# Kernel optimization log

Hardware: AMD Instinct MI355X
Metric: run time of the kernel (lower is better)

The kernel has to match this reference:

```python
import jax, jax.numpy as jnp
import numpy as np

D_MODEL = 1024
NUM_HEADS = 16
HEAD_DIM = D_MODEL // NUM_HEADS


def setup_inputs() -> dict:
    key = jax.random.key(0)
    ks = jax.random.split(key, 10)
    B, SQ, SKV = 4, 2048, 2048
    s = 1.0 / np.sqrt(D_MODEL)
    return {
        "query": jax.random.normal(ks[0], (B, SQ, D_MODEL), jnp.float32),
        "key_value": jax.random.normal(ks[1], (B, SKV, D_MODEL), jnp.float32),
        "Wq": jax.random.normal(ks[2], (D_MODEL, D_MODEL), jnp.float32) * s,
        "bq": jnp.zeros((D_MODEL,), jnp.float32),
        "Wk": jax.random.normal(ks[3], (D_MODEL, D_MODEL), jnp.float32) * s,
        "bk": jnp.zeros((D_MODEL,), jnp.float32),
        "Wv": jax.random.normal(ks[4], (D_MODEL, D_MODEL), jnp.float32) * s,
        "bv": jnp.zeros((D_MODEL,), jnp.float32),
        "Wo": jax.random.normal(ks[5], (D_MODEL, D_MODEL), jnp.float32) * s,
        "bo": jnp.zeros((D_MODEL,), jnp.float32),
    }


def reference(query, key_value, Wq, bq, Wk, bk, Wv, bv, Wo, bo):
    B, SQ, _ = query.shape
    SKV = key_value.shape[1]
    H, Dh = NUM_HEADS, HEAD_DIM
    # projections (torch Linear: x @ W.T + b); split heads -> (B, H, S, Dh)
    Q = (query @ Wq.T + bq).reshape(B, SQ, H, Dh).transpose(0, 2, 1, 3)
    K = (key_value @ Wk.T + bk).reshape(B, SKV, H, Dh).transpose(0, 2, 1, 3)
    V = (key_value @ Wv.T + bv).reshape(B, SKV, H, Dh).transpose(0, 2, 1, 3)
    scale = jnp.asarray(np.sqrt(Dh), query.dtype)
    scores = jnp.einsum("bhqd,bhkd->bhqk", Q, K) / scale
    weights = jax.nn.softmax(scores, axis=-1)  # dropout is identity in eval
    attn = jnp.einsum("bhqk,bhkd->bhqd", weights, V)
    attn = attn.transpose(0, 2, 1, 3).reshape(B, SQ, H * Dh)
    return attn @ Wo.T + bo
```

## Files before the change

### kernel.cpp

```cpp
#include <hip/hip_runtime.h>

#define NH 16
#define DH 64
#define DM 1024
#define SEQ 2048
#define BATCH 4

typedef short s16x8 __attribute__((ext_vector_type(8)));
typedef float f32x4 __attribute__((ext_vector_type(4)));

__device__ __forceinline__ unsigned short f2bf(float f) {
  union { float f; unsigned int u; } v; v.f = f;
  unsigned int u = v.u;
  unsigned int r = (u + 0x7fffu + ((u >> 16) & 1u)) >> 16;
  return (unsigned short)r;
}

__device__ __forceinline__ unsigned int pkbf(float a, float b) {
#if __has_builtin(__builtin_amdgcn_cvt_pk_bf16_f32)
  typedef short v2s __attribute__((ext_vector_type(2)));
  v2s r = __builtin_amdgcn_cvt_pk_bf16_f32(a, b);
  union { v2s v; unsigned int u; } cv; cv.v = r;
  return cv.u;
#else
  return (unsigned int)f2bf(a) | ((unsigned int)f2bf(b) << 16);
#endif
}

__device__ __forceinline__ float fexp2(float x) {
#if __has_builtin(__builtin_amdgcn_exp2f)
  return __builtin_amdgcn_exp2f(x);
#else
  return exp2f(x);
#endif
}

__device__ __forceinline__ void gload_lds16(const void* g, void* l) {
  __builtin_amdgcn_global_load_lds(
      (const __attribute__((address_space(1))) unsigned int*)g,
      (__attribute__((address_space(3))) unsigned int*)l, 16, 0, 0);
}

__global__ void convert_all(const float* __restrict__ q, const float* __restrict__ kv,
                            const float* __restrict__ w0, const float* __restrict__ w1,
                            const float* __restrict__ w2, const float* __restrict__ w3,
                            unsigned short* __restrict__ oq, unsigned short* __restrict__ okv,
                            unsigned short* __restrict__ ow0, unsigned short* __restrict__ ow1,
                            unsigned short* __restrict__ ow2, unsigned short* __restrict__ ow3) {
  const int NQ4 = (BATCH * SEQ * DM) / 4;
  const int NW4 = (DM * DM) / 4;
  const int total = NQ4 * 2 + NW4 * 4;
  for (int i = blockIdx.x * blockDim.x + threadIdx.x; i < total;
       i += gridDim.x * blockDim.x) {
    const float* s; unsigned short* d; int off;
    if (i < NQ4)            { s = q;  d = oq;  off = i; }
    else if (i < 2 * NQ4)   { s = kv; d = okv; off = i - NQ4; }
    else {
      int j = i - 2 * NQ4; int wsel = j / NW4; off = j - wsel * NW4;
      s = (wsel == 0) ? w0 : (wsel == 1) ? w1 : (wsel == 2) ? w2 : w3;
      d = (wsel == 0) ? ow0 : (wsel == 1) ? ow1 : (wsel == 2) ? ow2 : ow3;
    }
    float4 v = *(const float4*)(s + (size_t)off * 4);
    ushort4 o;
    o.x = f2bf(v.x); o.y = f2bf(v.y); o.z = f2bf(v.z); o.w = f2bf(v.w);
    *(ushort4*)(d + (size_t)off * 4) = o;
  }
}

__device__ __forceinline__ void gemm_tile(const unsigned short* __restrict__ X,
                                          const unsigned short* __restrict__ Wt,
                                          unsigned short* As, unsigned short* Bs,
                                          int m0, int n0, f32x4 (*acc)[4]) {
  const int tid = threadIdx.x;
  const int wv_ = tid >> 6, lane = tid & 63;
  const int quad = lane >> 4, c = lane & 15;
  const int wm = (wv_ >> 1) * 64, wn = (wv_ & 1) * 64;
  const int srow = lane >> 3;
  const int scol = ((lane & 7) ^ srow) * 8;

  for (int kt = 0; kt < DM; kt += 64) {
#pragma unroll
    for (int i = 0; i < 4; ++i) {
      int reg = wv_ * 4 + i;
      gload_lds16(X + (size_t)(m0 + reg * 8 + srow) * DM + kt + scol,
                  (void*)(As + reg * 512));
      gload_lds16(Wt + (size_t)(n0 + reg * 8 + srow) * DM + kt + scol,
                  (void*)(Bs + reg * 512));
    }
    __syncthreads();
#pragma unroll
    for (int k2 = 0; k2 < 2; ++k2) {
      s16x8 a[4], b[4];
      int g = k2 * 4 + quad;
#pragma unroll
      for (int t = 0; t < 4; ++t)
        a[t] = *(const s16x8*)(As + (wm + t * 16 + c) * 64 + ((g ^ (c & 7)) * 8));
#pragma unroll
      for (int t = 0; t < 4; ++t)
        b[t] = *(const s16x8*)(Bs + (wn + t * 16 + c) * 64 + ((g ^ (c & 7)) * 8));
#pragma unroll
      for (int tm = 0; tm < 4; ++tm)
#pragma unroll
        for (int tn = 0; tn < 4; ++tn)
          acc[tm][tn] = __builtin_amdgcn_mfma_f32_16x16x32_bf16(
              a[tm], b[tn], acc[tm][tn], 0, 0, 0);
    }
    __syncthreads();
  }
}

__global__ __launch_bounds__(256)
void gemm_qkv(const unsigned short* __restrict__ Xq,
              const unsigned short* __restrict__ Xkv,
              const unsigned short* __restrict__ W0,
              const unsigned short* __restrict__ W1,
              const unsigned short* __restrict__ W2,
              const float* __restrict__ b0, const float* __restrict__ b1,
              const float* __restrict__ b2,
              unsigned short* __restrict__ OQ, unsigned short* __restrict__ OK_,
              unsigned short* __restrict__ OV) {
  __shared__ alignas(16) unsigned short As[128 * 64];
  __shared__ alignas(16) unsigned short Bs[128 * 64];
  const int m0 = blockIdx.x * 128;
  const int ysel = blockIdx.y >> 3;
  const int n0 = (blockIdx.y & 7) * 128;
  const unsigned short* X = (ysel == 0) ? Xq : Xkv;
  const unsigned short* Wt = (ysel == 0) ? W0 : (ysel == 1) ? W1 : W2;
  const float* bias = (ysel == 0) ? b0 : (ysel == 1) ? b1 : b2;
  unsigned short* Out = (ysel == 0) ? OQ : (ysel == 1) ? OK_ : OV;
  const float scale = (ysel == 0) ? 0.1803368801f : 1.0f;

  f32x4 acc[4][4] = {};
  gemm_tile(X, Wt, As, Bs, m0, n0, acc);

  const int tid = threadIdx.x;
  const int wv_ = tid >> 6, lane = tid & 63;
  const int quad = lane >> 4, c = lane & 15;
  const int wm = (wv_ >> 1) * 64, wn = (wv_ & 1) * 64;
#pragma unroll
  for (int tm = 0; tm < 4; ++tm) {
#pragma unroll
    for (int tn = 0; tn < 4; ++tn) {
      int n = n0 + wn + tn * 16 + c;
      float bv = bias[n];
      int m_base = m0 + wm + tm * 16 + quad * 4;
      if (ysel == 2) {
        int b_ = m_base >> 11, s_ = m_base & 2047, h_ = n >> 6, dh = n & 63;
        size_t idx = (((size_t)(b_ * NH + h_)) * DH + dh) * SEQ + s_;
        ushort4 o4;
        o4.x = f2bf(acc[tm][tn][0] + bv);
        o4.y = f2bf(acc[tm][tn][1] + bv);
        o4.z = f2bf(acc[tm][tn][2] + bv);
        o4.w = f2bf(acc[tm][tn][3] + bv);
        *(ushort4*)(&Out[idx]) = o4;
      } else {
#pragma unroll
        for (int p = 0; p < 4; ++p) {
          int m = m_base + p;
          float val = (acc[tm][tn][p] + bv) * scale;
          int b_ = m >> 11, s_ = m & 2047, h_ = n >> 6, dh = n & 63;
          size_t idx = (((size_t)(b_ * NH + h_)) * SEQ + s_) * DH + dh;
          Out[idx] = f2bf(val);
        }
      }
    }
  }
}

__global__ __launch_bounds__(256)
void gemm_o(const unsigned short* __restrict__ X,
            const unsigned short* __restrict__ Wt,
            const float* __restrict__ bias, float* __restrict__ Out) {
  __shared__ alignas(16) unsigned short As[128 * 64];
  __shared__ alignas(16) unsigned short Bs[128 * 64];
  const int m0 = blockIdx.x * 128;
  const int n0 = blockIdx.y * 128;
  f32x4 acc[4][4] = {};
  gemm_tile(X, Wt, As, Bs, m0, n0, acc);

  const int tid = threadIdx.x;
  const int wv_ = tid >> 6, lane = tid & 63;
  const int quad = lane >> 4, c = lane & 15;
  const int wm = (wv_ >> 1) * 64, wn = (wv_ & 1) * 64;
#pragma unroll
  for (int tm = 0; tm < 4; ++tm) {
#pragma unroll
    for (int tn = 0; tn < 4; ++tn) {
      int n = n0 + wn + tn * 16 + c;
      float bv = bias[n];
#pragma unroll
      for (int p = 0; p < 4; ++p) {
        int m = m0 + wm + tm * 16 + quad * 4 + p;
        Out[(size_t)m * DM + n] = acc[tm][tn][p] + bv;
      }
    }
  }
}

__global__ __launch_bounds__(256, 2)
void attn_kernel(const unsigned short* __restrict__ Qb,
                 const unsigned short* __restrict__ Kb,
                 const unsigned short* __restrict__ VTb,
                 unsigned short* __restrict__ Ob) {
  __shared__ alignas(16) unsigned short SM[16384];

  const int tid = threadIdx.x, wv_ = tid >> 6, lane = tid & 63;
  const int quad = lane >> 4, c = lane & 15;
  const int bh = blockIdx.x, qb = blockIdx.y;
  const unsigned short* Qp = Qb + (size_t)bh * SEQ * DH;
  const unsigned short* Kp = Kb + (size_t)bh * SEQ * DH;
  const unsigned short* Vp = VTb + (size_t)bh * DH * SEQ;
  const int wq0 = qb * 256 + wv_ * 64;

  s16x8 aq[4][2];
#pragma unroll
  for (int t = 0; t < 4; ++t)
#pragma unroll
    for (int k2 = 0; k2 < 2; ++k2)
      aq[t][k2] = *(const s16x8*)(Qp + (size_t)(wq0 + t * 16 + c) * DH +
                                  k2 * 32 + quad * 8);

  f32x4 ot[4][4] = {};
  float lsum[4] = {};

  const int srow = lane >> 3;
  const int schunk = (lane & 7) ^ srow;

#pragma unroll
  for (int i = 0; i < 2; ++i) {
    int reg = wv_ * 2 + i;
    gload_lds16(Kp + (size_t)(reg * 8 + srow) * DH + schunk * 8,
                (void*)(SM + reg * 512));
    gload_lds16(Vp + (size_t)(reg * 8 + srow) * SEQ + schunk * 8,
                (void*)(SM + 8192 + reg * 512));
  }

  for (int kt = 0; kt < SEQ; kt += 64) {
    const int cur = (kt >> 6) & 1;
    __syncthreads();
    if (kt + 64 < SEQ) {
      const int nxt = cur ^ 1;
#pragma unroll
      for (int i = 0; i < 2; ++i) {
        int reg = wv_ * 2 + i;
        gload_lds16(Kp + (size_t)(kt + 64 + reg * 8 + srow) * DH + schunk * 8,
                    (void*)(SM + nxt * 4096 + reg * 512));
        gload_lds16(Vp + (size_t)(reg * 8 + srow) * SEQ + kt + 64 + schunk * 8,
                    (void*)(SM + 8192 + nxt * 4096 + reg * 512));
      }
    }
    const unsigned short* K_ = SM + cur * 4096;
    const unsigned short* V_ = SM + 8192 + cur * 4096;

    f32x4 s[4][2][2] = {};
#pragma unroll
    for (int k2 = 0; k2 < 2; ++k2) {
      s16x8 ak[2][2];
#pragma unroll
      for (int jp = 0; jp < 2; ++jp)
#pragma unroll
        for (int h = 0; h < 2; ++h) {
          int r = jp * 32 + ((c >> 2) << 3) + h * 4 + (c & 3);
          int g = k2 * 4 + quad;
          ak[jp][h] = *(const s16x8*)(K_ + r * 64 + ((g ^ (r & 7)) * 8));
        }
#pragma unroll
      for (int t = 0; t < 4; ++t)
#pragma unroll
        for (int jp = 0; jp < 2; ++jp)
#pragma unroll
          for (int h = 0; h < 2; ++h)
            s[t][jp][h] = __builtin_amdgcn_mfma_f32_16x16x32_bf16(
                ak[jp][h], aq[t][k2], s[t][jp][h], 0, 0, 0);
    }

    s16x8 bp[4][2];
#pragma unroll
    for (int t = 0; t < 4; ++t)
#pragma unroll
      for (int jp = 0; jp < 2; ++jp) {
        float e00 = fexp2(s[t][jp][0][0]);
        float e01 = fexp2(s[t][jp][0][1]);
        float e02 = fexp2(s[t][jp][0][2]);
        float e03 = fexp2(s[t][jp][0][3]);
        float e10 = fexp2(s[t][jp][1][0]);
        float e11 = fexp2(s[t][jp][1][1]);
        float e12 = fexp2(s[t][jp][1][2]);
        float e13 = fexp2(s[t][jp][1][3]);
        lsum[t] += ((e00 + e01) + (e02 + e03)) + ((e10 + e11) + (e12 + e13));
        union { s16x8 v; unsigned int u[4]; } pk;
        pk.u[0] = pkbf(e00, e01);
        pk.u[1] = pkbf(e02, e03);
        pk.u[2] = pkbf(e10, e11);
        pk.u[3] = pkbf(e12, e13);
        bp[t][jp] = pk.v;
      }

#pragma unroll
    for (int jp = 0; jp < 2; ++jp)
#pragma unroll
      for (int dt = 0; dt < 4; ++dt) {
        int g = jp * 4 + quad;
        int r = dt * 16 + c;
        s16x8 av = *(const s16x8*)(V_ + r * 64 + ((g ^ (r & 7)) * 8));
#pragma unroll
        for (int t = 0; t < 4; ++t)
          ot[dt][t] = __builtin_amdgcn_mfma_f32_16x16x32_bf16(
              av, bp[t][jp], ot[dt][t], 0, 0, 0);
      }
  }

#pragma unroll
  for (int t = 0; t < 4; ++t) {
    lsum[t] += __shfl_xor(lsum[t], 16);
    lsum[t] += __shfl_xor(lsum[t], 32);
  }

  __syncthreads();

  const int b_ = bh >> 4, h_ = bh & 15;
  const int ql = lane >> 1, hf = lane & 1;
  unsigned short* Lq = SM + wv_ * (32 * 72);
#pragma unroll
  for (int half = 0; half < 2; ++half) {
    if (half) asm volatile("s_waitcnt lgkmcnt(0)" ::: "memory");
#pragma unroll
    for (int t2 = 0; t2 < 2; ++t2) {
      int t = half * 2 + t2;
      float inv = 1.0f / lsum[t];
#pragma unroll
      for (int dt = 0; dt < 4; ++dt) {
        unsigned int w01 = pkbf(ot[dt][t][0] * inv, ot[dt][t][1] * inv);
        unsigned int w23 = pkbf(ot[dt][t][2] * inv, ot[dt][t][3] * inv);
        unsigned short* p = Lq + (t2 * 16 + c) * 72 + dt * 16 + quad * 4;
        *(unsigned int*)(p) = w01;
        *(unsigned int*)(p + 2) = w23;
      }
    }
    const unsigned short* Lr = Lq + ql * 72 + hf * 32;
    unsigned short* Og = Ob + ((size_t)(b_ * SEQ + wq0 + half * 32 + ql)) * DM +
                         h_ * 64 + hf * 32;
#pragma unroll
    for (int j = 0; j < 4; ++j) {
      s16x8 v = *(const s16x8*)(Lr + j * 8);
      *(s16x8*)(Og + j * 8) = v;
    }
  }
}

extern "C" void kernel_launch(void* const* d_in, const int* in_sizes, int n_in,
                              void* d_out, int out_size, void* d_ws, size_t ws_size,
                              hipStream_t stream) {
  const float* q  = (const float*)d_in[0];
  const float* kv = (const float*)d_in[1];
  const float* Wq = (const float*)d_in[2];
  const float* bq = (const float*)d_in[3];
  const float* Wk = (const float*)d_in[4];
  const float* bk = (const float*)d_in[5];
  const float* Wv = (const float*)d_in[6];
  const float* bv = (const float*)d_in[7];
  const float* Wo = (const float*)d_in[8];
  const float* bo = (const float*)d_in[9];

  char* ws = (char*)d_ws;
  const size_t MB = 1024 * 1024;
  unsigned short* q_bf  = (unsigned short*)(ws);
  unsigned short* kv_bf = (unsigned short*)(ws + 16 * MB);
  unsigned short* wq_bf = (unsigned short*)(ws + 32 * MB);
  unsigned short* wk_bf = (unsigned short*)(ws + 34 * MB);
  unsigned short* wv_bf = (unsigned short*)(ws + 36 * MB);
  unsigned short* wo_bf = (unsigned short*)(ws + 38 * MB);
  unsigned short* Qb    = (unsigned short*)(ws + 40 * MB);
  unsigned short* Kb    = (unsigned short*)(ws + 56 * MB);
  unsigned short* VTb   = (unsigned short*)(ws + 72 * MB);
  unsigned short* attn  = (unsigned short*)(ws + 88 * MB);

  convert_all<<<2048, 256, 0, stream>>>(q, kv, Wq, Wk, Wv, Wo,
                                        q_bf, kv_bf, wq_bf, wk_bf, wv_bf, wo_bf);
  gemm_qkv<<<dim3(64, 24), 256, 0, stream>>>(q_bf, kv_bf, wq_bf, wk_bf, wv_bf,
                                             bq, bk, bv, Qb, Kb, VTb);
  attn_kernel<<<dim3(64, 8), 256, 0, stream>>>(Qb, Kb, VTb, attn);
  gemm_o<<<dim3(64, 8), 256, 0, stream>>>(attn, wo_bf, bo, (float*)d_out);
}
```

Before: 308.4 us.

## Remap workgroups per XCD, use 512-thread attention blocks, MFMA row sums

Launches the GEMM and attention kernels on 1-D grids and remaps workgroup IDs so that consecutive tiles sharing the same inputs land on the same XCD, aiming for better L2 reuse. The attention kernel now uses 512-thread blocks, each handling 512 queries, so every K/V tile loaded into shared memory serves twice as many query rows. Within a block, waves split the K and V loads by slab. The softmax row sum is now computed with an extra MFMA against a ones vector instead of scalar adds and cross-lane shuffles, which sums the bf16-rounded probabilities. The costs are higher register pressure under the new 512-thread launch bounds and a larger shared-memory array.

```diff
diff --git a/kernel.cpp b/kernel.cpp
--- a/kernel.cpp
+++ b/kernel.cpp
@@ -121,9 +121,12 @@
               unsigned short* __restrict__ OV) {
   __shared__ alignas(16) unsigned short As[128 * 64];
   __shared__ alignas(16) unsigned short Bs[128 * 64];
-  const int m0 = blockIdx.x * 128;
-  const int ysel = blockIdx.y >> 3;
-  const int n0 = (blockIdx.y & 7) * 128;
+  const int wg = blockIdx.x;
+  const int L = (wg & 7) * 192 + (wg >> 3);
+  const int m0 = (L & 63) * 128;
+  const int yy = L >> 6;
+  const int ysel = yy >> 3;
+  const int n0 = (yy & 7) * 128;
   const unsigned short* X = (ysel == 0) ? Xq : Xkv;
   const unsigned short* Wt = (ysel == 0) ? W0 : (ysel == 1) ? W1 : W2;
   const float* bias = (ysel == 0) ? b0 : (ysel == 1) ? b1 : b2;
@@ -173,8 +176,10 @@
             const float* __restrict__ bias, float* __restrict__ Out) {
   __shared__ alignas(16) unsigned short As[128 * 64];
   __shared__ alignas(16) unsigned short Bs[128 * 64];
-  const int m0 = blockIdx.x * 128;
-  const int n0 = blockIdx.y * 128;
+  const int wg = blockIdx.x;
+  const int L = (wg & 7) * 64 + (wg >> 3);
+  const int m0 = (L & 63) * 128;
+  const int n0 = (L >> 6) * 128;
   f32x4 acc[4][4] = {};
   gemm_tile(X, Wt, As, Bs, m0, n0, acc);
 
@@ -197,20 +202,22 @@
   }
 }
 
-__global__ __launch_bounds__(256, 2)
+__global__ __launch_bounds__(512, 2)
 void attn_kernel(const unsigned short* __restrict__ Qb,
                  const unsigned short* __restrict__ Kb,
                  const unsigned short* __restrict__ VTb,
                  unsigned short* __restrict__ Ob) {
-  __shared__ alignas(16) unsigned short SM[16384];
+  __shared__ alignas(16) unsigned short SM[18432];
 
   const int tid = threadIdx.x, wv_ = tid >> 6, lane = tid & 63;
   const int quad = lane >> 4, c = lane & 15;
-  const int bh = blockIdx.x, qb = blockIdx.y;
+  const int wg = blockIdx.x;
+  const int bh = (wg & 7) + 8 * ((wg >> 3) >> 2);
+  const int qb = (wg >> 3) & 3;
   const unsigned short* Qp = Qb + (size_t)bh * SEQ * DH;
   const unsigned short* Kp = Kb + (size_t)bh * SEQ * DH;
   const unsigned short* Vp = VTb + (size_t)bh * DH * SEQ;
-  const int wq0 = qb * 256 + wv_ * 64;
+  const int wq0 = qb * 512 + wv_ * 64;
 
   s16x8 aq[4][2];
 #pragma unroll
@@ -221,18 +228,29 @@
                                   k2 * 32 + quad * 8);
 
   f32x4 ot[4][4] = {};
-  float lsum[4] = {};
+  f32x4 lacc[4] = {};
+  s16x8 ones;
+  {
+    union { s16x8 v; unsigned short u[8]; } o_;
+#pragma unroll
+    for (int j = 0; j < 8; ++j) o_.u[j] = 0x3F80;
+    ones = o_.v;
+  }
 
   const int srow = lane >> 3;
   const int schunk = (lane & 7) ^ srow;
 
 #pragma unroll
   for (int i = 0; i < 2; ++i) {
-    int reg = wv_ * 2 + i;
-    gload_lds16(Kp + (size_t)(reg * 8 + srow) * DH + schunk * 8,
-                (void*)(SM + reg * 512));
-    gload_lds16(Vp + (size_t)(reg * 8 + srow) * SEQ + schunk * 8,
-                (void*)(SM + 8192 + reg * 512));
+    int slab = wv_ * 2 + i;
+    if (slab < 8) {
+      gload_lds16(Kp + (size_t)(slab * 8 + srow) * DH + schunk * 8,
+                  (void*)(SM + slab * 512));
+    } else {
+      int s2 = slab - 8;
+      gload_lds16(Vp + (size_t)(s2 * 8 + srow) * SEQ + schunk * 8,
+                  (void*)(SM + 8192 + s2 * 512));
+    }
   }
 
   for (int kt = 0; kt < SEQ; kt += 64) {
@@ -242,11 +260,15 @@
       const int nxt = cur ^ 1;
 #pragma unroll
       for (int i = 0; i < 2; ++i) {
-        int reg = wv_ * 2 + i;
-        gload_lds16(Kp + (size_t)(kt + 64 + reg * 8 + srow) * DH + schunk * 8,
-                    (void*)(SM + nxt * 4096 + reg * 512));
-        gload_lds16(Vp + (size_t)(reg * 8 + srow) * SEQ + kt + 64 + schunk * 8,
-                    (void*)(SM + 8192 + nxt * 4096 + reg * 512));
+        int slab = wv_ * 2 + i;
+        if (slab < 8) {
+          gload_lds16(Kp + (size_t)(kt + 64 + slab * 8 + srow) * DH + schunk * 8,
+                      (void*)(SM + nxt * 4096 + slab * 512));
+        } else {
+          int s2 = slab - 8;
+          gload_lds16(Vp + (size_t)(s2 * 8 + srow) * SEQ + kt + 64 + schunk * 8,
+                      (void*)(SM + 8192 + nxt * 4096 + s2 * 512));
+        }
       }
     }
     const unsigned short* K_ = SM + cur * 4096;
@@ -287,13 +309,14 @@
         float e11 = fexp2(s[t][jp][1][1]);
         float e12 = fexp2(s[t][jp][1][2]);
         float e13 = fexp2(s[t][jp][1][3]);
-        lsum[t] += ((e00 + e01) + (e02 + e03)) + ((e10 + e11) + (e12 + e13));
         union { s16x8 v; unsigned int u[4]; } pk;
         pk.u[0] = pkbf(e00, e01);
         pk.u[1] = pkbf(e02, e03);
         pk.u[2] = pkbf(e10, e11);
         pk.u[3] = pkbf(e12, e13);
         bp[t][jp] = pk.v;
+        lacc[t] = __builtin_amdgcn_mfma_f32_16x16x32_bf16(
+            ones, bp[t][jp], lacc[t], 0, 0, 0);
       }
 
 #pragma unroll
@@ -310,12 +333,6 @@
       }
   }
 
-#pragma unroll
-  for (int t = 0; t < 4; ++t) {
-    lsum[t] += __shfl_xor(lsum[t], 16);
-    lsum[t] += __shfl_xor(lsum[t], 32);
-  }
-
   __syncthreads();
 
   const int b_ = bh >> 4, h_ = bh & 15;
@@ -327,7 +344,7 @@
 #pragma unroll
     for (int t2 = 0; t2 < 2; ++t2) {
       int t = half * 2 + t2;
-      float inv = 1.0f / lsum[t];
+      float inv = 1.0f / lacc[t][0];
 #pragma unroll
       for (int dt = 0; dt < 4; ++dt) {
         unsigned int w01 = pkbf(ot[dt][t][0] * inv, ot[dt][t][1] * inv);
@@ -377,8 +394,8 @@
 
   convert_all<<<2048, 256, 0, stream>>>(q, kv, Wq, Wk, Wv, Wo,
                                         q_bf, kv_bf, wq_bf, wk_bf, wv_bf, wo_bf);
-  gemm_qkv<<<dim3(64, 24), 256, 0, stream>>>(q_bf, kv_bf, wq_bf, wk_bf, wv_bf,
-                                             bq, bk, bv, Qb, Kb, VTb);
-  attn_kernel<<<dim3(64, 8), 256, 0, stream>>>(Qb, Kb, VTb, attn);
-  gemm_o<<<dim3(64, 8), 256, 0, stream>>>(attn, wo_bf, bo, (float*)d_out);
-}
+  gemm_qkv<<<dim3(1536), 256, 0, stream>>>(q_bf, kv_bf, wq_bf, wk_bf, wv_bf,
+                                           bq, bk, bv, Qb, Kb, VTb);
+  attn_kernel<<<dim3(256), 512, 0, stream>>>(Qb, Kb, VTb, attn);
+  gemm_o<<<dim3(512), 256, 0, stream>>>(attn, wo_bf, bo, (float*)d_out);
+}
```

Result: slower. 325.7 us (+5.6%).
